# Kernel optimization log

Hardware: AMD Instinct MI355X
Metric: run time of the kernel (lower is better)

## Reference

```python
import jax, jax.numpy as jnp
import numpy as np

WBITS = 4
ABITS = 8
OBITS = 8


def fwht(x):
    """Normalized fast Walsh-Hadamard transform along the last axis (n power of 2).
    Equivalent to matmul_hadU with had_K = I, K = 1 (n = 4096 = 2^12)."""
    shape = x.shape
    n = shape[-1]
    x = x.reshape(-1, n)
    h = 1
    while h < n:
        x = x.reshape(-1, n // (2 * h), 2, h)
        a, b = x[:, :, 0, :], x[:, :, 1, :]
        x = jnp.concatenate([a + b, a - b], axis=-1).reshape(-1, n)
        h *= 2
    inv_sqrt_n = jnp.asarray(1.0 / np.sqrt(n), x.dtype)
    return (x * inv_sqrt_n).reshape(shape)


def sym_fake_quant(t, bits, axis):
    """Symmetric min-max RTN fake quantization (per-channel for weights,
    per-token for activations)."""
    qmax = jnp.asarray(2.0 ** (bits - 1) - 1.0, t.dtype)
    scale = jnp.max(jnp.abs(t), axis=axis, keepdims=True) / qmax
    scale = jnp.maximum(scale, jnp.asarray(1e-8, t.dtype))
    q = jnp.clip(jnp.round(t / scale), -qmax, qmax)
    return q * scale


def setup_inputs() -> dict:
    key = jax.random.key(0)
    k1, k2, k3 = jax.random.split(key, 3)
    B, S, DIN, DOUT = 4, 2048, 4096, 4096
    return {
        "input": jax.random.normal(k1, (B, S, DIN), dtype=jnp.float32),
        "weight": jax.random.normal(k2, (DOUT, DIN), dtype=jnp.float32) * 0.02,
        "bias": jax.random.normal(k3, (DOUT,), dtype=jnp.float32) * 0.01,
    }


def reference(input, weight, bias):
    # online full Hadamard rotation of activations
    x = fwht(input)
    # activation quant (per-token, symmetric int8 fake-quant)
    x = sym_fake_quant(x, ABITS, axis=-1)
    # weight quant (per-output-channel, symmetric int4 fake-quant)
    w = sym_fake_quant(weight, WBITS, axis=-1)
    # F.linear: x @ w.T + b
    out = jnp.einsum("bsi,oi->bso", x, w) + bias
    # output quant (per-token, symmetric int8 fake-quant)
    out = sym_fake_quant(out, OBITS, axis=-1)
    return out
```

## Files before the change

### kernel.cpp

```cpp
#include <hip/hip_runtime.h>
#include <hip/hip_bf16.h>

#define DIN 4096
#define DOUT 4096
#define NROWS 8192

typedef int i32x4 __attribute__((ext_vector_type(4)));

__device__ __forceinline__ float block_absmax(float m, float* red) {
  #pragma unroll
  for (int off = 32; off > 0; off >>= 1)
    m = fmaxf(m, __shfl_down(m, off));
  const int tid = threadIdx.x;
  if ((tid & 63) == 0) red[tid >> 6] = m;
  __syncthreads();
  return fmaxf(fmaxf(red[0], red[1]), fmaxf(red[2], red[3]));
}

__global__ __launch_bounds__(256) void fused_quant_kernel(
    const float* __restrict__ in, const float* __restrict__ w,
    char* __restrict__ qx, char* __restrict__ qw,
    float* __restrict__ sx, float* __restrict__ sw) {
  __shared__ float lds[4352];
  __shared__ float red[4];
  const int tid = threadIdx.x;

  if (blockIdx.x < NROWS) {
    const size_t row = blockIdx.x;
    const int th = tid >> 4, tl = tid & 15;
    float v[16];
    const float4* src = (const float4*)(in + row * DIN);
    #pragma unroll
    for (int k = 0; k < 4; ++k) {
      float4 f = src[tid * 4 + k];
      v[4 * k + 0] = f.x; v[4 * k + 1] = f.y;
      v[4 * k + 2] = f.z; v[4 * k + 3] = f.w;
    }
    #pragma unroll
    for (int hb = 1; hb < 16; hb <<= 1)
      #pragma unroll
      for (int j = 0; j < 16; ++j)
        if (!(j & hb)) {
          float a0 = v[j], b0 = v[j | hb];
          v[j] = a0 + b0; v[j | hb] = a0 - b0;
        }
    #pragma unroll
    for (int j = 0; j < 16; ++j) lds[17 * tid + j] = v[j];
    __syncthreads();
    #pragma unroll
    for (int j = 0; j < 16; ++j) v[j] = lds[272 * th + 17 * j + tl];
    #pragma unroll
    for (int hb = 1; hb < 16; hb <<= 1)
      #pragma unroll
      for (int j = 0; j < 16; ++j)
        if (!(j & hb)) {
          float a0 = v[j], b0 = v[j | hb];
          v[j] = a0 + b0; v[j | hb] = a0 - b0;
        }
    #pragma unroll
    for (int j = 0; j < 16; ++j) lds[272 * th + 17 * j + tl] = v[j];
    __syncthreads();
    #pragma unroll
    for (int j = 0; j < 16; ++j) v[j] = lds[272 * j + 17 * th + tl];
    #pragma unroll
    for (int hb = 1; hb < 16; hb <<= 1)
      #pragma unroll
      for (int j = 0; j < 16; ++j)
        if (!(j & hb)) {
          float a0 = v[j], b0 = v[j | hb];
          v[j] = a0 + b0; v[j | hb] = a0 - b0;
        }
    float m = 0.0f;
    #pragma unroll
    for (int j = 0; j < 16; ++j) m = fmaxf(m, fabsf(v[j]));
    #pragma unroll
    for (int j = 0; j < 16; ++j) lds[272 * j + 17 * th + tl] = v[j];
    float mx = block_absmax(m, red) * 0.015625f;
    float scale = fmaxf(mx / 127.0f, 1e-8f);
    if (tid == 0) sx[row] = scale;
    const float rs = 1.0f / scale;
    char pk[16];
    #pragma unroll
    for (int j = 0; j < 16; ++j) {
      float q = fminf(fmaxf(rintf((lds[17 * tid + j] * 0.015625f) * rs), -127.f),
                      127.f);
      pk[j] = (char)q;
    }
    *(int4*)(qx + row * DIN + (size_t)tid * 16) = *(const int4*)pk;
  } else {
    const size_t row = blockIdx.x - NROWS;
    const float4* src = (const float4*)(w + row * DIN);
    float4* b4 = (float4*)lds;
    float m = 0.0f;
    for (int i = tid; i < DIN / 4; i += 256) {
      float4 v = src[i];
      b4[i] = v;
      m = fmaxf(m, fmaxf(fmaxf(fabsf(v.x), fabsf(v.y)),
                         fmaxf(fabsf(v.z), fabsf(v.w))));
    }
    float mx = block_absmax(m, red);
    float scale = fmaxf(mx / 7.0f, 1e-8f);
    if (tid == 0) sw[row] = scale;
    char* dst = qw + row * DIN;
    const float rs = 1.0f / scale;
    for (int i0 = tid * 4; i0 < DIN; i0 += 1024) {
      char4 pk;
      float q0 = fminf(fmaxf(rintf(lds[i0 + 0] * rs), -7.f), 7.f);
      float q1 = fminf(fmaxf(rintf(lds[i0 + 1] * rs), -7.f), 7.f);
      float q2 = fminf(fmaxf(rintf(lds[i0 + 2] * rs), -7.f), 7.f);
      float q3 = fminf(fmaxf(rintf(lds[i0 + 3] * rs), -7.f), 7.f);
      pk.x = (char)q0; pk.y = (char)q1; pk.z = (char)q2; pk.w = (char)q3;
      *(char4*)(dst + i0) = pk;
    }
  }
}

__global__ __launch_bounds__(512, 4) void gemm_kernel(
    const char* __restrict__ A,
    const char* __restrict__ Bt,
    const float* __restrict__ sx, const float* __restrict__ sw,
    const float* __restrict__ bias, float* __restrict__ out) {
  __shared__ char lds[49152];
  const int tid = threadIdx.x;
  const int lane = tid & 63;
  const int wid = tid >> 6;
  const int wr = wid >> 1;
  const int wc = wid & 1;
  int bid = blockIdx.x;
  int swz = (bid & 7) * 128 + (bid >> 3);
  const size_t row0 = (size_t)(swz >> 5) * 256;
  const size_t col0 = (size_t)(swz & 31) * 128;
  const int g16 = lane >> 4;

  i32x4 acc[4][4] = {};
  i32x4 fb[4];
  i32x4 fa;

#define STAGE_UNIT(MAT, GROW0, KT, LBASE)                                     \
  {                                                                           \
    int rr = wid * 16 + (lane >> 2);                                          \
    int cc = (KT) * 64 + ((((lane & 3) ^ ((rr >> 1) & 3))) << 4);             \
    const char* src = (MAT) + ((GROW0) + rr) * (size_t)DIN + cc;              \
    __builtin_amdgcn_global_load_lds(                                         \
        (const __attribute__((address_space(1))) void*)src,                   \
        (__attribute__((address_space(3))) void*)(lds + (LBASE) +             \
                                                  wid * 1024),                \
        16, 0, 0);                                                            \
  }
#define STAGE_A(P, HALF, KT) \
  STAGE_UNIT(A, row0 + (HALF) * 128, KT, (P) * 16384 + (HALF) * 8192)
#define STAGE_B(P, KT) STAGE_UNIT(Bt, col0, KT, 32768 + (P) * 8192)

#define DS_FA(Q, P)                                                           \
  {                                                                           \
    int ar = (Q) * 64 + wr * 16 + (lane & 15);                                \
    fa = *(const i32x4*)(lds + (P) * 16384 + ar * 64 +                        \
                         ((g16 ^ ((ar >> 1) & 3)) << 4));                     \
  }
#define DS_FB(P)                                                              \
  {                                                                           \
    _Pragma("unroll")                                                         \
    for (int nn = 0; nn < 4; ++nn) {                                          \
      int br = wc * 64 + nn * 16 + (lane & 15);                               \
      fb[nn] = *(const i32x4*)(lds + 32768 + (P) * 8192 + br * 64 +           \
                               ((g16 ^ ((br >> 1) & 3)) << 4));               \
    }                                                                         \
  }
#define MFMA4(Q)                                                              \
  {                                                                           \
    __builtin_amdgcn_s_setprio(1);                                            \
    _Pragma("unroll")                                                         \
    for (int nn = 0; nn < 4; ++nn)                                            \
      acc[Q][nn] = __builtin_amdgcn_mfma_i32_16x16x64_i8(                     \
          fa, fb[nn], acc[Q][nn], 0, 0, 0);                                   \
    __builtin_amdgcn_s_setprio(0);                                            \
  }
#define BAR() __builtin_amdgcn_s_barrier()
#define WAIT_LGKM0() asm volatile("s_waitcnt lgkmcnt(0)" ::: "memory")

  STAGE_B(0, 0); STAGE_A(0, 0, 0); STAGE_A(0, 1, 0);
  STAGE_B(1, 1); STAGE_A(1, 0, 1);
  asm volatile("s_waitcnt vmcnt(2)" ::: "memory");
  BAR();

  #pragma unroll 1
  for (int i = 0; i < 32; ++i) {
    const int a = 2 * i, b = 2 * i + 1;
    const bool nl = (i < 31);
    DS_FA(0, 0); DS_FB(0);
    STAGE_A(1, 1, b);
    BAR(); WAIT_LGKM0();
    MFMA4(0);
    BAR();
    DS_FA(1, 0);
    if (nl) STAGE_B(0, a + 2);
    BAR(); WAIT_LGKM0();
    MFMA4(1);
    BAR();
    DS_FA(2, 0);
    if (nl) STAGE_A(0, 0, a + 2);
    BAR(); WAIT_LGKM0();
    MFMA4(2);
    BAR();
    DS_FA(3, 0);
    BAR(); WAIT_LGKM0();
    MFMA4(3);
    if (nl) { asm volatile("s_waitcnt vmcnt(2)" ::: "memory"); }
    else    { asm volatile("s_waitcnt vmcnt(0)" ::: "memory"); }
    BAR();
    DS_FA(0, 1); DS_FB(1);
    if (nl) STAGE_A(0, 1, a + 2);
    BAR(); WAIT_LGKM0();
    MFMA4(0);
    BAR();
    DS_FA(1, 1);
    if (nl) STAGE_B(1, b + 2);
    BAR(); WAIT_LGKM0();
    MFMA4(1);
    BAR();
    DS_FA(2, 1);
    if (nl) STAGE_A(1, 0, b + 2);
    BAR(); WAIT_LGKM0();
    MFMA4(2);
    BAR();
    DS_FA(3, 1);
    BAR(); WAIT_LGKM0();
    MFMA4(3);
    if (nl) { asm volatile("s_waitcnt vmcnt(2)" ::: "memory"); }
    BAR();
  }

  #pragma unroll
  for (int q = 0; q < 4; ++q) {
    #pragma unroll
    for (int nn = 0; nn < 4; ++nn) {
      size_t gc = col0 + wc * 64 + nn * 16 + (lane & 15);
      float swc = sw[gc], bc = bias[gc];
      #pragma unroll
      for (int j = 0; j < 4; ++j) {
        size_t gr = row0 + q * 64 + wr * 16 + (g16 << 2) + j;
        out[gr * DOUT + gc] = (float)acc[q][nn][j] * (sx[gr] * swc) + bc;
      }
    }
  }
#undef STAGE_UNIT
#undef STAGE_A
#undef STAGE_B
#undef DS_FA
#undef DS_FB
#undef MFMA4
#undef BAR
#undef WAIT_LGKM0
}

__global__ __launch_bounds__(256) void rowquant_kernel(float* __restrict__ out) {
  __shared__ float red[4];
  const int tid = threadIdx.x;
  const size_t row = blockIdx.x;
  float4* g4 = (float4*)(out + row * DOUT);
  float4 v[4];
  float m = 0.0f;
  #pragma unroll
  for (int k = 0; k < 4; ++k) {
    v[k] = g4[tid + k * 256];
    m = fmaxf(m, fmaxf(fmaxf(fabsf(v[k].x), fabsf(v[k].y)),
                       fmaxf(fabsf(v[k].z), fabsf(v[k].w))));
  }
  float mx = block_absmax(m, red);
  float scale = fmaxf(mx / 127.0f, 1e-8f);
  #pragma unroll
  for (int k = 0; k < 4; ++k) {
    float4 w = v[k];
    w.x = fminf(fmaxf(rintf(w.x / scale), -127.0f), 127.0f) * scale;
    w.y = fminf(fmaxf(rintf(w.y / scale), -127.0f), 127.0f) * scale;
    w.z = fminf(fmaxf(rintf(w.z / scale), -127.0f), 127.0f) * scale;
    w.w = fminf(fmaxf(rintf(w.w / scale), -127.0f), 127.0f) * scale;
    g4[tid + k * 256] = w;
  }
}

extern "C" void kernel_launch(void* const* d_in, const int* in_sizes, int n_in,
                              void* d_out, int out_size, void* d_ws, size_t ws_size,
                              hipStream_t stream) {
  (void)in_sizes; (void)n_in; (void)out_size; (void)ws_size;
  const float* input = (const float*)d_in[0];
  const float* weight = (const float*)d_in[1];
  const float* bias = (const float*)d_in[2];
  float* out = (float*)d_out;
  char* ws = (char*)d_ws;
  char* qx = ws;
  char* qw = ws + ((size_t)32 << 20);
  float* sx = (float*)(ws + ((size_t)48 << 20));
  float* sw = (float*)(ws + ((size_t)48 << 20) + ((size_t)32 << 10));

  fused_quant_kernel<<<NROWS + DOUT, 256, 0, stream>>>(input, weight, qx, qw,
                                                       sx, sw);
  gemm_kernel<<<1024, 512, 0, stream>>>(qx, qw, sx, sw, bias, out);
  rowquant_kernel<<<NROWS, 256, 0, stream>>>(out);
}
```

Baseline: 239.9 us.

## Reshape GEMM tile to 128x256 with swapped MFMA operands and vectorized epilogue

Changes the GEMM block tile from 256 rows x 128 cols to 128 rows x 256 cols, with waves laid out 2x4 instead of 4x2. Each wave now loads two A fragments and issues eight MFMAs per phase, which halves the number of barrier-separated phases per k-step. The MFMA operands are swapped so each lane's accumulators hold four consecutive output columns, which lets the epilogue use float4 stores and float4 loads of scale and bias. The LDS staging layout and prefetch order are reworked to match, and fewer barriers per k-step also means less room to overlap loads with MFMAs.

```diff
diff --git a/kernel.cpp b/kernel.cpp
--- a/kernel.cpp
+++ b/kernel.cpp
@@ -124,17 +124,17 @@
   const int tid = threadIdx.x;
   const int lane = tid & 63;
   const int wid = tid >> 6;
-  const int wr = wid >> 1;
-  const int wc = wid & 1;
+  const int wr = wid >> 2;
+  const int wc = wid & 3;
   int bid = blockIdx.x;
   int swz = (bid & 7) * 128 + (bid >> 3);
-  const size_t row0 = (size_t)(swz >> 5) * 256;
-  const size_t col0 = (size_t)(swz & 31) * 128;
+  const size_t row0 = (size_t)(swz >> 4) * 128;
+  const size_t col0 = (size_t)(swz & 15) * 256;
   const int g16 = lane >> 4;
 
   i32x4 acc[4][4] = {};
   i32x4 fb[4];
-  i32x4 fa;
+  i32x4 fa[2];
 
 #define STAGE_UNIT(MAT, GROW0, KT, LBASE)                                     \
   {                                                                           \
@@ -147,39 +147,44 @@
                                                   wid * 1024),                \
         16, 0, 0);                                                            \
   }
-#define STAGE_A(P, HALF, KT) \
-  STAGE_UNIT(A, row0 + (HALF) * 128, KT, (P) * 16384 + (HALF) * 8192)
-#define STAGE_B(P, KT) STAGE_UNIT(Bt, col0, KT, 32768 + (P) * 8192)
-
-#define DS_FA(Q, P)                                                           \
-  {                                                                           \
-    int ar = (Q) * 64 + wr * 16 + (lane & 15);                                \
-    fa = *(const i32x4*)(lds + (P) * 16384 + ar * 64 +                        \
-                         ((g16 ^ ((ar >> 1) & 3)) << 4));                     \
+#define STAGE_A(P, KT) STAGE_UNIT(A, row0, KT, (P) * 8192)
+#define STAGE_B(P, H, KT) \
+  STAGE_UNIT(Bt, col0 + (H) * 128, KT, 16384 + (P) * 16384 + (H) * 8192)
+
+#define DS_FA2(M0, P)                                                         \
+  {                                                                           \
+    _Pragma("unroll")                                                         \
+    for (int m2 = 0; m2 < 2; ++m2) {                                          \
+      int ar = wr * 64 + ((M0) + m2) * 16 + (lane & 15);                      \
+      fa[m2] = *(const i32x4*)(lds + (P) * 8192 + ar * 64 +                   \
+                               ((g16 ^ ((ar >> 1) & 3)) << 4));               \
+    }                                                                         \
   }
 #define DS_FB(P)                                                              \
   {                                                                           \
     _Pragma("unroll")                                                         \
     for (int nn = 0; nn < 4; ++nn) {                                          \
       int br = wc * 64 + nn * 16 + (lane & 15);                               \
-      fb[nn] = *(const i32x4*)(lds + 32768 + (P) * 8192 + br * 64 +           \
+      fb[nn] = *(const i32x4*)(lds + 16384 + (P) * 16384 + br * 64 +          \
                                ((g16 ^ ((br >> 1) & 3)) << 4));               \
     }                                                                         \
   }
-#define MFMA4(Q)                                                              \
+#define MFMA8(M0)                                                             \
   {                                                                           \
     __builtin_amdgcn_s_setprio(1);                                            \
     _Pragma("unroll")                                                         \
-    for (int nn = 0; nn < 4; ++nn)                                            \
-      acc[Q][nn] = __builtin_amdgcn_mfma_i32_16x16x64_i8(                     \
-          fa, fb[nn], acc[Q][nn], 0, 0, 0);                                   \
+    for (int m2 = 0; m2 < 2; ++m2)                                            \
+      _Pragma("unroll")                                                       \
+      for (int nn = 0; nn < 4; ++nn)                                          \
+        acc[(M0) + m2][nn] = __builtin_amdgcn_mfma_i32_16x16x64_i8(           \
+            fb[nn], fa[m2], acc[(M0) + m2][nn], 0, 0, 0);                     \
     __builtin_amdgcn_s_setprio(0);                                            \
   }
 #define BAR() __builtin_amdgcn_s_barrier()
 #define WAIT_LGKM0() asm volatile("s_waitcnt lgkmcnt(0)" ::: "memory")
 
-  STAGE_B(0, 0); STAGE_A(0, 0, 0); STAGE_A(0, 1, 0);
-  STAGE_B(1, 1); STAGE_A(1, 0, 1);
+  STAGE_B(0, 0, 0); STAGE_B(0, 1, 0); STAGE_A(0, 0);
+  STAGE_B(1, 0, 1); STAGE_B(1, 1, 1);
   asm volatile("s_waitcnt vmcnt(2)" ::: "memory");
   BAR();
 
@@ -187,68 +192,55 @@
   for (int i = 0; i < 32; ++i) {
     const int a = 2 * i, b = 2 * i + 1;
     const bool nl = (i < 31);
-    DS_FA(0, 0); DS_FB(0);
-    STAGE_A(1, 1, b);
-    BAR(); WAIT_LGKM0();
-    MFMA4(0);
-    BAR();
-    DS_FA(1, 0);
-    if (nl) STAGE_B(0, a + 2);
-    BAR(); WAIT_LGKM0();
-    MFMA4(1);
-    BAR();
-    DS_FA(2, 0);
-    if (nl) STAGE_A(0, 0, a + 2);
-    BAR(); WAIT_LGKM0();
-    MFMA4(2);
-    BAR();
-    DS_FA(3, 0);
-    BAR(); WAIT_LGKM0();
-    MFMA4(3);
+    DS_FB(0); DS_FA2(0, 0);
+    STAGE_A(1, b);
+    BAR(); WAIT_LGKM0();
+    MFMA8(0);
+    BAR();
+    DS_FA2(2, 0);
+    if (nl) { STAGE_B(0, 0, a + 2); STAGE_B(0, 1, a + 2); }
+    BAR(); WAIT_LGKM0();
+    MFMA8(2);
     if (nl) { asm volatile("s_waitcnt vmcnt(2)" ::: "memory"); }
     else    { asm volatile("s_waitcnt vmcnt(0)" ::: "memory"); }
     BAR();
-    DS_FA(0, 1); DS_FB(1);
-    if (nl) STAGE_A(0, 1, a + 2);
-    BAR(); WAIT_LGKM0();
-    MFMA4(0);
-    BAR();
-    DS_FA(1, 1);
-    if (nl) STAGE_B(1, b + 2);
-    BAR(); WAIT_LGKM0();
-    MFMA4(1);
-    BAR();
-    DS_FA(2, 1);
-    if (nl) STAGE_A(1, 0, b + 2);
-    BAR(); WAIT_LGKM0();
-    MFMA4(2);
-    BAR();
-    DS_FA(3, 1);
-    BAR(); WAIT_LGKM0();
-    MFMA4(3);
+    DS_FB(1); DS_FA2(0, 1);
+    if (nl) STAGE_A(0, a + 2);
+    BAR(); WAIT_LGKM0();
+    MFMA8(0);
+    BAR();
+    DS_FA2(2, 1);
+    if (nl) { STAGE_B(1, 0, b + 2); STAGE_B(1, 1, b + 2); }
+    BAR(); WAIT_LGKM0();
+    MFMA8(2);
     if (nl) { asm volatile("s_waitcnt vmcnt(2)" ::: "memory"); }
     BAR();
   }
 
   #pragma unroll
-  for (int q = 0; q < 4; ++q) {
+  for (int mm = 0; mm < 4; ++mm) {
+    size_t gr = row0 + wr * 64 + mm * 16 + (lane & 15);
+    float sxr = sx[gr];
+    float* orow = out + gr * DOUT;
     #pragma unroll
     for (int nn = 0; nn < 4; ++nn) {
-      size_t gc = col0 + wc * 64 + nn * 16 + (lane & 15);
-      float swc = sw[gc], bc = bias[gc];
-      #pragma unroll
-      for (int j = 0; j < 4; ++j) {
-        size_t gr = row0 + q * 64 + wr * 16 + (g16 << 2) + j;
-        out[gr * DOUT + gc] = (float)acc[q][nn][j] * (sx[gr] * swc) + bc;
-      }
+      size_t gc0 = col0 + wc * 64 + nn * 16 + ((lane >> 4) << 2);
+      float4 swv = *(const float4*)(sw + gc0);
+      float4 bv = *(const float4*)(bias + gc0);
+      float4 o;
+      o.x = (float)acc[mm][nn][0] * (sxr * swv.x) + bv.x;
+      o.y = (float)acc[mm][nn][1] * (sxr * swv.y) + bv.y;
+      o.z = (float)acc[mm][nn][2] * (sxr * swv.z) + bv.z;
+      o.w = (float)acc[mm][nn][3] * (sxr * swv.w) + bv.w;
+      *(float4*)(orow + gc0) = o;
     }
   }
 #undef STAGE_UNIT
 #undef STAGE_A
 #undef STAGE_B
-#undef DS_FA
+#undef DS_FA2
 #undef DS_FB
-#undef MFMA4
+#undef MFMA8
 #undef BAR
 #undef WAIT_LGKM0
 }
```

Result: no change. 243.1 us (+1.3%).
